# Kernel tuning notes

Hardware: AMD Instinct MI355X
Metric: run time of the kernel (lower is better)

Reference implementation:

```python
import jax, jax.numpy as jnp
import numpy as np

B, C, H, W = 4, 256, 64, 64
CP = C // 4  # embedding_channels, k=4 hardcoded
# branch index -> (key-stream i, query/value-stream j); streams: 0=t,1=b,2=m
IIDX = np.array([0, 0, 0, 1, 1, 1, 2, 2, 2])  # which stream feeds k
JIDX = np.array([0, 1, 2, 0, 1, 2, 0, 1, 2])  # which stream feeds q and v


def setup_inputs() -> dict:
    key = jax.random.key(0)
    ks = jax.random.split(key, 6)
    scale = 0.05
    return {
        "t": jax.random.normal(ks[0], (B, C, H, W), jnp.float32),
        "b": jax.random.normal(ks[1], (B, C, H, W), jnp.float32),
        "m": jax.random.normal(ks[2], (B, C, H, W), jnp.float32),
        "W_qkv": jax.random.normal(ks[3], (9, C, C), jnp.float32) * scale,
        "W_red": jax.random.normal(ks[4], (9, CP, C), jnp.float32) * scale,
        "W_rec": jax.random.normal(ks[5], (9, C, CP), jnp.float32) * scale,
    }


def _pool(x):
    # ChannelAttention: global avg pool + global max pool -> [B, C']
    return jnp.mean(x, axis=(2, 3)) + jnp.max(x, axis=(2, 3))


def _channel_attention(q, k, v, w_red, w_rec):
    # q,k,v: [B,C,H,W]; w_red: [C',C]; w_rec: [C,C']
    ori = q + k + v
    red = lambda x: jax.nn.relu(jnp.einsum("bchw,ec->behw", x, w_red))
    qr, kr, vr = red(q), red(k), red(v)
    f = _pool(kr)  # key   -> [B,C']
    g = _pool(qr)  # query -> [B,C']
    h = _pool(vr)  # value -> [B,C']
    # s = f^T g : [B,C',C']; softmax over dim=1 (rows), per torch nn.Softmax(dim=1)
    s = f[:, :, None] * g[:, None, :]
    beta = jax.nn.softmax(s, axis=1)
    vout = jnp.einsum("bi,bij->bj", h, beta)  # [B,C']
    # recovery 1x1 conv on [B,C',1,1]; bilinear upsample from 1x1 == broadcast
    o = jax.nn.sigmoid(jnp.einsum("be,ce->bc", vout, w_rec))  # [B,C]
    return o[:, :, None, None] * ori


def reference(t, b, m, W_qkv, W_red, W_rec):
    x = jnp.stack([t, b, m])  # [3,B,C,H,W]
    Wp = W_qkv.reshape(3, 3, C, C)  # [stream, (q,k,v), C_out, C_in]
    proj = jnp.einsum("sbchw,sjec->sjbehw", x, Wp)  # [3,3,B,C,H,W]
    Q, K, V = proj[:, 0], proj[:, 1], proj[:, 2]  # each [3,B,C,H,W]
    q9, k9, v9 = Q[JIDX], K[IIDX], V[JIDX]  # [9,B,C,H,W]
    outs = jax.vmap(_channel_attention)(q9, k9, v9, W_red, W_rec)
    return outs.sum(axis=0)
```

## Files before the change

kernel.cpp:

```cpp
#include <hip/hip_runtime.h>

#define Bn 4
#define Cn 256
#define HWn 4096
#define CPn 64
#define MP 640

typedef unsigned short u16;
typedef unsigned int u32;
typedef unsigned long long u64;

using short8  = __attribute__((ext_vector_type(8))) short;
using floatx4 = __attribute__((ext_vector_type(4))) float;

static __device__ __forceinline__ u16 f2bf(float f) {
    union { float f; u32 u; } v; v.f = f;
    u32 r = (v.u + 0x7FFFu + ((v.u >> 16) & 1u)) >> 16;
    return (u16)r;
}

static __device__ __forceinline__ void gld16(const u16* g, u16* l) {
    __builtin_amdgcn_global_load_lds(
        (const __attribute__((address_space(1))) u32*)g,
        (__attribute__((address_space(3))) u32*)l, 16, 0, 0);
}


__global__ __launch_bounds__(256) void prep(
    const float* __restrict__ Tt, const float* __restrict__ Bt, const float* __restrict__ Mt,
    const float* __restrict__ Wqkv, const float* __restrict__ Wred,
    u16* __restrict__ xT, u16* __restrict__ CWp)
{
    __shared__ __align__(16) u16 T[64][72];
    __shared__ float As[16][64];
    __shared__ float Bs[16][64];
    const int t = threadIdx.x;

    if (blockIdx.z < 3) {
        const int s  = blockIdx.z, b = blockIdx.y;
        const int ct = blockIdx.x & 3, hwt = blockIdx.x >> 2;
        const int c0 = ct * 64, hw0 = hwt * 64;
        const float* X = (s == 0 ? Tt : (s == 1 ? Bt : Mt)) + (size_t)b * Cn * HWn;

        const int cl = t >> 2, q = t & 3;
        const float* src = X + (size_t)(c0 + cl) * HWn + hw0 + q * 16;
        #pragma unroll
        for (int u = 0; u < 4; ++u) {
            const float4 v = *(const float4*)(src + u * 4);
            u64 pk = (u64)f2bf(v.x) | ((u64)f2bf(v.y) << 16) |
                     ((u64)f2bf(v.z) << 32) | ((u64)f2bf(v.w) << 48);
            *(u64*)&T[cl][q * 16 + u * 4] = pk;
        }
        __syncthreads();

        const int wl = t >> 2;
        u16* dst = xT + ((size_t)((s * Bn + b) * HWn) + hw0 + wl) * Cn + c0 + q * 16;
        #pragma unroll
        for (int u = 0; u < 2; ++u) {
            u32 w0 = (u32)T[q * 16 + u * 8 + 0][wl] | ((u32)T[q * 16 + u * 8 + 1][wl] << 16);
            u32 w1 = (u32)T[q * 16 + u * 8 + 2][wl] | ((u32)T[q * 16 + u * 8 + 3][wl] << 16);
            u32 w2 = (u32)T[q * 16 + u * 8 + 4][wl] | ((u32)T[q * 16 + u * 8 + 5][wl] << 16);
            u32 w3 = (u32)T[q * 16 + u * 8 + 6][wl] | ((u32)T[q * 16 + u * 8 + 7][wl] << 16);
            uint4 pk = {w0, w1, w2, w3};
            *(uint4*)(dst + u * 8) = pk;
        }
        return;
    }

    const int lin = blockIdx.y * 256 + blockIdx.x;
    if (lin >= 108) return;
    const int c0  = (lin & 3) * 64;
    const int rest = lin >> 2;
    const int y9 = rest % 9, s = rest / 9;
    const int tt = y9 / 3, m3 = y9 % 3;
    const int idx = (tt == 1) ? (3 * s + m3) : (3 * m3 + s);

    const float* A  = Wred + (size_t)idx * CPn * Cn;
    const float* Bm = Wqkv + (size_t)(3 * s + tt) * Cn * Cn;

    const int ty = t >> 4, tx = t & 15;
    float acc[4][4] = {};

    for (int k0 = 0; k0 < Cn; k0 += 16) {
        {
            const int r = t >> 2, eq = (t & 3) * 4;
            const float4 a = *(const float4*)(A + (size_t)r * Cn + k0 + eq);
            As[eq + 0][r] = a.x; As[eq + 1][r] = a.y; As[eq + 2][r] = a.z; As[eq + 3][r] = a.w;
        }
        {
            const int r = t >> 4, cq = (t & 15) * 4;
            *(float4*)(&Bs[r][cq]) = *(const float4*)(Bm + (size_t)(k0 + r) * Cn + c0 + cq);
        }
        __syncthreads();
        #pragma unroll
        for (int k = 0; k < 16; ++k) {
            const float4 a4 = *(const float4*)(&As[k][ty * 4]);
            const float4 b4 = *(const float4*)(&Bs[k][tx * 4]);
            const float a[4] = {a4.x, a4.y, a4.z, a4.w};
            const float bb[4] = {b4.x, b4.y, b4.z, b4.w};
            #pragma unroll
            for (int i = 0; i < 4; ++i)
                #pragma unroll
                for (int j = 0; j < 4; ++j)
                    acc[i][j] = fmaf(a[i], bb[j], acc[i][j]);
        }
        __syncthreads();
    }

    u16* outp = CWp + (size_t)s * MP * Cn;
    #pragma unroll
    for (int i = 0; i < 4; ++i) {
        const int row = tt * 192 + m3 * 64 + ty * 4 + i;
        unsigned long long pk =
            (unsigned long long)f2bf(acc[i][0]) |
            ((unsigned long long)f2bf(acc[i][1]) << 16) |
            ((unsigned long long)f2bf(acc[i][2]) << 32) |
            ((unsigned long long)f2bf(acc[i][3]) << 48);
        *(unsigned long long*)(outp + (size_t)row * Cn + c0 + tx * 4) = pk;
    }
}

#define NSUB 8

__global__ __launch_bounds__(256, 2) void redpool_mfma(
    const u16* __restrict__ xT, const u16* __restrict__ CWp,
    float* __restrict__ Psum, float* __restrict__ Pmax)
{
    const int s   = blockIdx.z;
    const int mt  = blockIdx.x >> 5, nch = blockIdx.x & 31;
    const int m0  = mt * 128;
    const int nbase = nch * 512;

    const u16* Ap = CWp + (size_t)s * MP * Cn;
    const u16* Bp = xT + (size_t)s * Bn * HWn * Cn;

    __shared__ __align__(16) u16 Bs[2][32 * 512];

    const int t = threadIdx.x;
    const int w = t >> 6, lane = t & 63;
    const int l15 = lane & 15, q = lane >> 4;
    const int wr = w >> 1, wc = w & 1;

    short8 af[4][8];
    {
        const u16* Arow = Ap + (size_t)(m0 + wr * 64 + l15) * Cn + q * 8;
        #pragma unroll
        for (int i = 0; i < 4; ++i)
            #pragma unroll
            for (int kk = 0; kk < 8; ++kk)
                af[i][kk] = *(const short8*)(Arow + (size_t)(i * 16) * Cn + kk * 32);
    }

    auto stageB = [&](int it, int buf) {
        const u16* Bsrc = Bp + (size_t)(nbase + it * 64 + l15) * Cn + q * 8;
        #pragma unroll
        for (int pi = 0; pi < 8; ++pi) {
            const int p = w * 8 + pi;
            gld16(Bsrc + (size_t)((p >> 3) * 16) * Cn + (p & 7) * 32, &Bs[buf][p * 512]);
        }
    };
    stageB(0, 0);

    float rs[4][4] = {};
    float rm[4][4] = {};

    for (int it = 0; it < NSUB; ++it) {
        __syncthreads();
        if (it + 1 < NSUB) stageB(it + 1, (it + 1) & 1);
        const u16* bb = Bs[it & 1];

        floatx4 acc[4][2] = {};
        __builtin_amdgcn_s_setprio(1);
        #pragma unroll
        for (int kk = 0; kk < 8; ++kk) {
            short8 bf[2];
            #pragma unroll
            for (int j = 0; j < 2; ++j)
                bf[j] = *(const short8*)&bb[((wc * 2 + j) * 8 + kk) * 512 + lane * 8];
            #pragma unroll
            for (int i = 0; i < 4; ++i)
                #pragma unroll
                for (int j = 0; j < 2; ++j)
                    acc[i][j] = __builtin_amdgcn_mfma_f32_16x16x32_bf16(af[i][kk], bf[j], acc[i][j], 0, 0, 0);
        }
        __builtin_amdgcn_s_setprio(0);
        #pragma unroll
        for (int i = 0; i < 4; ++i)
            #pragma unroll
            for (int r = 0; r < 4; ++r) {
                const float v0 = fmaxf(acc[i][0][r], 0.f);
                const float v1 = fmaxf(acc[i][1][r], 0.f);
                rs[i][r] += v0 + v1;
                rm[i][r] = fmaxf(rm[i][r], fmaxf(v0, v1));
            }
    }

    #pragma unroll
    for (int i = 0; i < 4; ++i)
        #pragma unroll
        for (int r = 0; r < 4; ++r) {
            #pragma unroll
            for (int off = 1; off < 16; off <<= 1) {
                rs[i][r] += __shfl_xor(rs[i][r], off);
                rm[i][r] = fmaxf(rm[i][r], __shfl_xor(rm[i][r], off));
            }
        }

    __syncthreads();
    float* Lsum = (float*)&Bs[0][0];
    float* Lmax = Lsum + 256;
    if (l15 == 0) {
        #pragma unroll
        for (int i = 0; i < 4; ++i)
            #pragma unroll
            for (int r = 0; r < 4; ++r) {
                const int row = wr * 64 + i * 16 + q * 4 + r;
                Lsum[wc * 128 + row] = rs[i][r];
                Lmax[wc * 128 + row] = rm[i][r];
            }
    }
    __syncthreads();
    if (t < 128) {
        const int R = m0 + t;
        const size_t o = ((size_t)s * MP + R) * 32 + nch;
        Psum[o] = Lsum[t] + Lsum[128 + t];
        Pmax[o] = fmaxf(Lmax[t], Lmax[128 + t]);
    }
}

__global__ __launch_bounds__(64) void attn_small(
    const float* __restrict__ Psum, const float* __restrict__ Pmax,
    float* __restrict__ vout)
{
    const int idx = blockIdx.x / Bn;
    const int bb  = blockIdx.x % Bn;
    __shared__ float ff[CPn], gg[CPn], hh[CPn];
    const int t = threadIdx.x;

    float v[3];
    #pragma unroll
    for (int tt = 0; tt < 3; ++tt) {
        const int s_ = (tt == 1) ? idx / 3 : idx % 3;
        const int m3 = (tt == 1) ? idx % 3 : idx / 3;
        const int R  = tt * 192 + m3 * 64 + t;
        const size_t base = ((size_t)s_ * MP + R) * 32 + bb * 8;
        float sm = 0.f, mx = 0.f;
        #pragma unroll
        for (int u = 0; u < 8; ++u) {
            sm += Psum[base + u];
            mx = fmaxf(mx, Pmax[base + u]);
        }
        v[tt] = sm * (1.0f / HWn) + mx;
    }
    gg[t] = v[0];
    ff[t] = v[1];
    hh[t] = v[2];
    __syncthreads();

    const float gj = gg[t];
    float mx = -1e30f;
    for (int i = 0; i < CPn; ++i) mx = fmaxf(mx, ff[i] * gj);
    float den = 0.f, num = 0.f;
    for (int i = 0; i < CPn; ++i) {
        const float e = expf(ff[i] * gj - mx);
        den += e;
        num += hh[i] * e;
    }
    vout[((size_t)idx * Bn + bb) * CPn + t] = num / den;
}

__global__ __launch_bounds__(256) void build_M(
    const float* __restrict__ Wqkv, const float* __restrict__ Wrec,
    const float* __restrict__ vout, u16* __restrict__ Mm)
{
    const int s = blockIdx.x >> 8, m = blockIdx.x & 255;
    const int b = blockIdx.y;
    const int t = threadIdx.x;
    __shared__ float cc[2];

    if (t < CPn) {
        float d[6];
        #pragma unroll
        for (int j = 0; j < 6; ++j) {
            const int idx = (j < 3) ? (s + 3 * j) : (3 * s + (j - 3));
            d[j] = vout[((size_t)idx * Bn + b) * CPn + t] *
                   Wrec[((size_t)idx * Cn + m) * CPn + t];
        }
        #pragma unroll
        for (int off = 32; off >= 1; off >>= 1)
            #pragma unroll
            for (int j = 0; j < 6; ++j)
                d[j] += __shfl_xor(d[j], off);
        if (t == 0) {
            float cA = 0.f, cK = 0.f;
            #pragma unroll
            for (int j = 0; j < 3; ++j) {
                cA += 1.0f / (1.0f + expf(-d[j]));
                cK += 1.0f / (1.0f + expf(-d[j + 3]));
            }
            cc[0] = cA; cc[1] = cK;
        }
    }
    __syncthreads();
    const float cA = cc[0], cK = cc[1];
    const float wq = Wqkv[((size_t)(3 * s + 0) * Cn + m) * Cn + t];
    const float wk = Wqkv[((size_t)(3 * s + 1) * Cn + m) * Cn + t];
    const float wv = Wqkv[((size_t)(3 * s + 2) * Cn + m) * Cn + t];
    Mm[((size_t)(b * 256 + m)) * 768 + s * 256 + t] = f2bf(cA * (wq + wv) + cK * wk);
}

__global__ __launch_bounds__(256, 1) void final_mfma(
    const u16* __restrict__ xT, const u16* __restrict__ Mm,
    float* __restrict__ out)
{
    const int b  = blockIdx.y;
    const int mt = blockIdx.x >> 5, nt = blockIdx.x & 31;
    const int m0 = mt * 128, n0 = nt * 128;

    __shared__ __align__(16) u16 As[2][32 * 512];
    __shared__ __align__(16) u16 Bs[2][32 * 512];

    const int t = threadIdx.x;
    const int w = t >> 6, lane = t & 63;
    const int l15 = lane & 15, q = lane >> 4;
    const int rb = (w >> 1) * 64, cb = (w & 1) * 64;

    auto stage = [&](int it, int buf) {
        const int k0 = it * 128;
        const int s = k0 >> 8, c0 = k0 & 255;
        const u16* Asrc = Mm + (size_t)(b * 256 + m0 + l15) * 768 + k0 + q * 8;
        const u16* Bsrc = xT + ((size_t)((s * Bn + b) * HWn) + n0 + l15) * Cn + c0 + q * 8;
        #pragma unroll
        for (int pi = 0; pi < 8; ++pi) {
            const int p = w * 8 + pi;
            const size_t roff = (size_t)((p >> 2) * 16);
            gld16(Asrc + roff * 768 + (p & 3) * 32, &As[buf][p * 512]);
            gld16(Bsrc + roff * Cn + (p & 3) * 32, &Bs[buf][p * 512]);
        }
    };
    stage(0, 0);

    floatx4 acc[4][4] = {};

    for (int it = 0; it < 6; ++it) {
        __syncthreads();
        if (it + 1 < 6) stage(it + 1, (it + 1) & 1);
        const u16* as = As[it & 1];
        const u16* bs = Bs[it & 1];
        #pragma unroll
        for (int kk = 0; kk < 4; ++kk) {
            short8 af[4], bf[4];
            #pragma unroll
            for (int i = 0; i < 4; ++i)
                af[i] = *(const short8*)&as[((((w >> 1) * 4 + i) << 2) + kk) * 512 + lane * 8];
            #pragma unroll
            for (int j = 0; j < 4; ++j)
                bf[j] = *(const short8*)&bs[((((w & 1) * 4 + j) << 2) + kk) * 512 + lane * 8];
            #pragma unroll
            for (int i = 0; i < 4; ++i)
                #pragma unroll
                for (int j = 0; j < 4; ++j)
                    acc[i][j] = __builtin_amdgcn_mfma_f32_16x16x32_bf16(af[i], bf[j], acc[i][j], 0, 0, 0);
        }
    }

    #pragma unroll
    for (int i = 0; i < 4; ++i)
        #pragma unroll
        for (int j = 0; j < 4; ++j)
            #pragma unroll
            for (int r = 0; r < 4; ++r) {
                const int row = m0 + rb + i * 16 + q * 4 + r;
                const int col = n0 + cb + j * 16 + l15;
                out[((size_t)(b * 256) + row) * HWn + col] = acc[i][j][r];
            }
}

extern "C" void kernel_launch(void* const* d_in, const int* in_sizes, int n_in,
                              void* d_out, int out_size, void* d_ws, size_t ws_size,
                              hipStream_t stream)
{
    const float* Tt   = (const float*)d_in[0];
    const float* Bt   = (const float*)d_in[1];
    const float* Mt   = (const float*)d_in[2];
    const float* Wqkv = (const float*)d_in[3];
    const float* Wred = (const float*)d_in[4];
    const float* Wrec = (const float*)d_in[5];
    float* out = (float*)d_out;

    unsigned char* p = (unsigned char*)d_ws;
    u16* xT = (u16*)p;            p += (size_t)3 * Bn * HWn * Cn * 2;
    u16* Mm = (u16*)p;            p += (size_t)Bn * 256 * 768 * 2;
    u16* CWp = (u16*)p;           p += (size_t)3 * MP * Cn * 2;
    float* Psum = (float*)p;      p += (size_t)3 * MP * 32 * 4;
    float* Pmax = (float*)p;      p += (size_t)3 * MP * 32 * 4;
    float* vout = (float*)p;      p += (size_t)9 * Bn * CPn * 4;

    prep        <<<dim3(256, Bn, 4), 256, 0, stream>>>(Tt, Bt, Mt, Wqkv, Wred, xT, CWp);
    redpool_mfma<<<dim3(160, 1, 3),  256, 0, stream>>>(xT, CWp, Psum, Pmax);
    attn_small  <<<9 * Bn,            64, 0, stream>>>(Psum, Pmax, vout);
    build_M     <<<dim3(768, Bn),    256, 0, stream>>>(Wqkv, Wrec, vout, Mm);
    final_mfma  <<<dim3(64, Bn),     256, 0, stream>>>(xT, Mm, out);
}
```

Before: 173.0 us.

## Fuse fp32-to-bf16 conversion into reduction-pool kernel, reading raw inputs directly

The reduction-pool kernel now reads the fp32 input streams directly, converts them to bf16 and transposes them through shared memory into an MFMA-ready layout, then runs all five M-tiles against that 64-pixel slab. This removes the dependence on the prep kernel's transposed xT buffer for this stage, and lets each block reuse its loaded slab across all projection rows. Partial sums now go out per 64-pixel tile (256 chunks), so attn_small reads more partials with vectorized loads. Prep still writes xT for final_mfma, so the full-size transpose is not removed. The new kernel runs one block per CU, reloads the A weights from global memory for every M-tile, and drops double-buffered overlap.

```diff
diff --git a/kernel.cpp b/kernel.cpp
--- a/kernel.cpp
+++ b/kernel.cpp
@@ -5,6 +5,7 @@
 #define HWn 4096
 #define CPn 64
 #define MP 640
+#define NCH 256
 
 typedef unsigned short u16;
 typedef unsigned int u32;
@@ -120,111 +121,101 @@
     }
 }
 
-#define NSUB 8
-
-__global__ __launch_bounds__(256, 2) void redpool_mfma(
-    const u16* __restrict__ xT, const u16* __restrict__ CWp,
+__global__ __launch_bounds__(256, 1) void redpool_fused(
+    const float* __restrict__ Tt, const float* __restrict__ Bt, const float* __restrict__ Mt,
+    const u16* __restrict__ CWp,
     float* __restrict__ Psum, float* __restrict__ Pmax)
 {
-    const int s   = blockIdx.z;
-    const int mt  = blockIdx.x >> 5, nch = blockIdx.x & 31;
-    const int m0  = mt * 128;
-    const int nbase = nch * 512;
-
-    const u16* Ap = CWp + (size_t)s * MP * Cn;
-    const u16* Bp = xT + (size_t)s * Bn * HWn * Cn;
-
-    __shared__ __align__(16) u16 Bs[2][32 * 512];
-
+    __shared__ __align__(16) u16 PN[32 * 512];
+    __shared__ __align__(16) u16 T[64][72];
     const int t = threadIdx.x;
     const int w = t >> 6, lane = t & 63;
     const int l15 = lane & 15, q = lane >> 4;
-    const int wr = w >> 1, wc = w & 1;
-
-    short8 af[4][8];
-    {
-        const u16* Arow = Ap + (size_t)(m0 + wr * 64 + l15) * Cn + q * 8;
-        #pragma unroll
-        for (int i = 0; i < 4; ++i)
-            #pragma unroll
-            for (int kk = 0; kk < 8; ++kk)
-                af[i][kk] = *(const short8*)(Arow + (size_t)(i * 16) * Cn + kk * 32);
-    }
-
-    auto stageB = [&](int it, int buf) {
-        const u16* Bsrc = Bp + (size_t)(nbase + it * 64 + l15) * Cn + q * 8;
-        #pragma unroll
-        for (int pi = 0; pi < 8; ++pi) {
-            const int p = w * 8 + pi;
-            gld16(Bsrc + (size_t)((p >> 3) * 16) * Cn + (p & 7) * 32, &Bs[buf][p * 512]);
-        }
-    };
-    stageB(0, 0);
-
-    float rs[4][4] = {};
-    float rm[4][4] = {};
-
-    for (int it = 0; it < NSUB; ++it) {
-        __syncthreads();
-        if (it + 1 < NSUB) stageB(it + 1, (it + 1) & 1);
-        const u16* bb = Bs[it & 1];
-
-        floatx4 acc[4][2] = {};
-        __builtin_amdgcn_s_setprio(1);
-        #pragma unroll
-        for (int kk = 0; kk < 8; ++kk) {
-            short8 bf[2];
-            #pragma unroll
-            for (int j = 0; j < 2; ++j)
-                bf[j] = *(const short8*)&bb[((wc * 2 + j) * 8 + kk) * 512 + lane * 8];
-            #pragma unroll
-            for (int i = 0; i < 4; ++i)
-                #pragma unroll
-                for (int j = 0; j < 2; ++j)
-                    acc[i][j] = __builtin_amdgcn_mfma_f32_16x16x32_bf16(af[i][kk], bf[j], acc[i][j], 0, 0, 0);
-        }
-        __builtin_amdgcn_s_setprio(0);
-        #pragma unroll
-        for (int i = 0; i < 4; ++i)
-            #pragma unroll
-            for (int r = 0; r < 4; ++r) {
-                const float v0 = fmaxf(acc[i][0][r], 0.f);
-                const float v1 = fmaxf(acc[i][1][r], 0.f);
-                rs[i][r] += v0 + v1;
-                rm[i][r] = fmaxf(rm[i][r], fmaxf(v0, v1));
-            }
-    }
-
-    #pragma unroll
-    for (int i = 0; i < 4; ++i)
-        #pragma unroll
-        for (int r = 0; r < 4; ++r) {
-            #pragma unroll
-            for (int off = 1; off < 16; off <<= 1) {
-                rs[i][r] += __shfl_xor(rs[i][r], off);
-                rm[i][r] = fmaxf(rm[i][r], __shfl_xor(rm[i][r], off));
-            }
-        }
-
-    __syncthreads();
-    float* Lsum = (float*)&Bs[0][0];
-    float* Lmax = Lsum + 256;
-    if (l15 == 0) {
-        #pragma unroll
-        for (int i = 0; i < 4; ++i)
-            #pragma unroll
-            for (int r = 0; r < 4; ++r) {
-                const int row = wr * 64 + i * 16 + q * 4 + r;
-                Lsum[wc * 128 + row] = rs[i][r];
-                Lmax[wc * 128 + row] = rm[i][r];
-            }
-    }
-    __syncthreads();
-    if (t < 128) {
-        const int R = m0 + t;
-        const size_t o = ((size_t)s * MP + R) * 32 + nch;
-        Psum[o] = Lsum[t] + Lsum[128 + t];
-        Pmax[o] = fmaxf(Lmax[t], Lmax[128 + t]);
+    const int b = blockIdx.x >> 6, hwt = blockIdx.x & 63;
+    const int hw0 = hwt * 64;
+    const int cl = t >> 2, qq = t & 3;
+
+    #pragma unroll 1
+    for (int s = 0; s < 3; ++s) {
+        const float* X = (s == 0 ? Tt : (s == 1 ? Bt : Mt)) + (size_t)b * Cn * HWn;
+
+        #pragma unroll 1
+        for (int ct = 0; ct < 4; ++ct) {
+            const float* src = X + (size_t)(ct * 64 + cl) * HWn + hw0 + qq * 16;
+            #pragma unroll
+            for (int u = 0; u < 4; ++u) {
+                const float4 v = *(const float4*)(src + u * 4);
+                u64 pk = (u64)f2bf(v.x) | ((u64)f2bf(v.y) << 16) |
+                         ((u64)f2bf(v.z) << 32) | ((u64)f2bf(v.w) << 48);
+                *(u64*)&T[cl][qq * 16 + u * 4] = pk;
+            }
+            __syncthreads();
+            #pragma unroll
+            for (int u = 0; u < 2; ++u) {
+                u32 w0 = (u32)T[qq*16+u*8+0][cl] | ((u32)T[qq*16+u*8+1][cl] << 16);
+                u32 w1 = (u32)T[qq*16+u*8+2][cl] | ((u32)T[qq*16+u*8+3][cl] << 16);
+                u32 w2 = (u32)T[qq*16+u*8+4][cl] | ((u32)T[qq*16+u*8+5][cl] << 16);
+                u32 w3 = (u32)T[qq*16+u*8+6][cl] | ((u32)T[qq*16+u*8+7][cl] << 16);
+                uint4 pk4 = {w0, w1, w2, w3};
+                const int c8 = ct * 8 + qq * 2 + u;
+                const int addr = (((cl >> 4) * 8 + (c8 >> 2)) << 9) +
+                                 (((c8 & 3) * 16 + (cl & 15)) << 3);
+                *(uint4*)&PN[addr] = pk4;
+            }
+            __syncthreads();
+        }
+
+        #pragma unroll 1
+        for (int mt = 0; mt < 5; ++mt) {
+            const u16* Arow = CWp + (size_t)s * MP * Cn +
+                              (size_t)(mt * 128 + w * 32 + l15) * Cn + q * 8;
+            short8 af[2][8];
+            #pragma unroll
+            for (int i = 0; i < 2; ++i)
+                #pragma unroll
+                for (int kk = 0; kk < 8; ++kk)
+                    af[i][kk] = *(const short8*)(Arow + (size_t)(i * 16) * Cn + kk * 32);
+
+            floatx4 acc[2][4] = {};
+            __builtin_amdgcn_s_setprio(1);
+            #pragma unroll
+            for (int kk = 0; kk < 8; ++kk) {
+                short8 bf[4];
+                #pragma unroll
+                for (int j = 0; j < 4; ++j)
+                    bf[j] = *(const short8*)&PN[((j * 8 + kk) << 9) + lane * 8];
+                #pragma unroll
+                for (int i = 0; i < 2; ++i)
+                    #pragma unroll
+                    for (int j = 0; j < 4; ++j)
+                        acc[i][j] = __builtin_amdgcn_mfma_f32_16x16x32_bf16(af[i][kk], bf[j], acc[i][j], 0, 0, 0);
+            }
+            __builtin_amdgcn_s_setprio(0);
+
+            #pragma unroll
+            for (int i = 0; i < 2; ++i)
+                #pragma unroll
+                for (int r = 0; r < 4; ++r) {
+                    float sm = 0.f, mx = 0.f;
+                    #pragma unroll
+                    for (int j = 0; j < 4; ++j) {
+                        const float v = fmaxf(acc[i][j][r], 0.f);
+                        sm += v; mx = fmaxf(mx, v);
+                    }
+                    #pragma unroll
+                    for (int off = 1; off < 16; off <<= 1) {
+                        sm += __shfl_xor(sm, off);
+                        mx = fmaxf(mx, __shfl_xor(mx, off));
+                    }
+                    if (l15 == 0) {
+                        const int R = mt * 128 + w * 32 + i * 16 + q * 4 + r;
+                        const size_t o = ((size_t)s * MP + R) * NCH + blockIdx.x;
+                        Psum[o] = sm;
+                        Pmax[o] = mx;
+                    }
+                }
+        }
+        __syncthreads();
     }
 }
 
@@ -243,12 +234,16 @@
         const int s_ = (tt == 1) ? idx / 3 : idx % 3;
         const int m3 = (tt == 1) ? idx % 3 : idx / 3;
         const int R  = tt * 192 + m3 * 64 + t;
-        const size_t base = ((size_t)s_ * MP + R) * 32 + bb * 8;
+        const size_t base = ((size_t)s_ * MP + R) * NCH + bb * 64;
+        const float4* P4 = (const float4*)(Psum + base);
+        const float4* M4 = (const float4*)(Pmax + base);
         float sm = 0.f, mx = 0.f;
         #pragma unroll
-        for (int u = 0; u < 8; ++u) {
-            sm += Psum[base + u];
-            mx = fmaxf(mx, Pmax[base + u]);
+        for (int u = 0; u < 16; ++u) {
+            const float4 a = P4[u];
+            sm += (a.x + a.y) + (a.z + a.w);
+            const float4 c = M4[u];
+            mx = fmaxf(mx, fmaxf(fmaxf(c.x, c.y), fmaxf(c.z, c.w)));
         }
         v[tt] = sm * (1.0f / HWn) + mx;
     }
@@ -392,13 +387,13 @@
     u16* xT = (u16*)p;            p += (size_t)3 * Bn * HWn * Cn * 2;
     u16* Mm = (u16*)p;            p += (size_t)Bn * 256 * 768 * 2;
     u16* CWp = (u16*)p;           p += (size_t)3 * MP * Cn * 2;
-    float* Psum = (float*)p;      p += (size_t)3 * MP * 32 * 4;
-    float* Pmax = (float*)p;      p += (size_t)3 * MP * 32 * 4;
+    float* Psum = (float*)p;      p += (size_t)3 * MP * NCH * 4;
+    float* Pmax = (float*)p;      p += (size_t)3 * MP * NCH * 4;
     float* vout = (float*)p;      p += (size_t)9 * Bn * CPn * 4;
 
-    prep        <<<dim3(256, Bn, 4), 256, 0, stream>>>(Tt, Bt, Mt, Wqkv, Wred, xT, CWp);
-    redpool_mfma<<<dim3(160, 1, 3),  256, 0, stream>>>(xT, CWp, Psum, Pmax);
-    attn_small  <<<9 * Bn,            64, 0, stream>>>(Psum, Pmax, vout);
-    build_M     <<<dim3(768, Bn),    256, 0, stream>>>(Wqkv, Wrec, vout, Mm);
-    final_mfma  <<<dim3(64, Bn),     256, 0, stream>>>(xT, Mm, out);
-}
+    prep         <<<dim3(256, Bn, 4), 256, 0, stream>>>(Tt, Bt, Mt, Wqkv, Wred, xT, CWp);
+    redpool_fused<<<dim3(256),        256, 0, stream>>>(Tt, Bt, Mt, CWp, Psum, Pmax);
+    attn_small   <<<9 * Bn,            64, 0, stream>>>(Psum, Pmax, vout);
+    build_M      <<<dim3(768, Bn),    256, 0, stream>>>(Wqkv, Wrec, vout, Mm);
+    final_mfma   <<<dim3(64, Bn),     256, 0, stream>>>(xT, Mm, out);
+}
```

Result: slower. 211.0 us (+22.0%).
